# Optimization experiments

Hardware: AMD Instinct MI355X
Metric: run time of the kernel (lower is better)

Reference implementation:

```python
import jax, jax.numpy as jnp
import numpy as np

N = 4096
D_MODEL = 512


def setup_inputs() -> dict:
    key = jax.random.key(0)
    ks = jax.random.split(key, 5)
    scale = 1.0 / np.sqrt(D_MODEL)
    return {
        "x": jax.random.normal(ks[0], (N, D_MODEL), dtype=jnp.float32),
        "Wq": jax.random.normal(ks[1], (D_MODEL, D_MODEL), dtype=jnp.float32) * scale,
        "Wk": jax.random.normal(ks[2], (D_MODEL, D_MODEL), dtype=jnp.float32) * scale,
        "Wv": jax.random.normal(ks[3], (D_MODEL, D_MODEL), dtype=jnp.float32) * scale,
        "Ws": jax.random.normal(ks[4], (1, D_MODEL), dtype=jnp.float32) * scale,
    }


def reference(x, Wq, Wk, Wv, Ws):
    # x: [N, d]; torch nn.Linear(bias=False) computes x @ W.T
    Q = x @ Wq.T  # [N, d]
    K = x @ Wk.T  # [N, d]
    V = x @ Wv.T  # [N, d]
    sigma = jnp.clip(x @ Ws.T, 0.001, 1.0)  # [N, 1]

    # prior association: Gaussian kernel over |i - j| with per-row sigma
    pos = jnp.arange(sigma.shape[0], dtype=jnp.float32)
    diff = jnp.abs(pos[:, None] - pos[None, :])  # [N, N]
    gaussian = jnp.exp(-0.5 * (diff / sigma) ** 2) / jnp.sqrt(2.0 * jnp.pi * sigma)
    P = gaussian / (gaussian.sum(axis=1, keepdims=True) + 1e-8)

    scale = jnp.sqrt(jnp.float32(x.shape[-1]))
    S = jax.nn.softmax((Q @ K.T) / scale, axis=-1)  # [N, N]
    Z = S @ V  # [N, d]
    return Z, P, S
```

## Files before the change

### kernel.cpp

```cpp
#include <hip/hip_runtime.h>
#include <math.h>

#define N_TOK 4096
#define DM 512

typedef _Float16 f16x8 __attribute__((ext_vector_type(8)));
typedef _Float16 f16x4 __attribute__((ext_vector_type(4)));
typedef float f32x4 __attribute__((ext_vector_type(4)));

__device__ __forceinline__ void async_ld16(const ushort* g, ushort* l) {
  __builtin_amdgcn_global_load_lds(
      (const __attribute__((address_space(1))) void*)g,
      (__attribute__((address_space(3))) void*)l, 16, 0, 0);
}

__global__ __launch_bounds__(256) void pack_sigma(
    const float* __restrict__ x, const float* __restrict__ Wq,
    const float* __restrict__ Wk, const float* __restrict__ Wv,
    const float* __restrict__ Ws, _Float16* __restrict__ x16,
    _Float16* __restrict__ Wc16, float* __restrict__ sg) {
  const int b = blockIdx.x;
  const int t = threadIdx.x;
  if (b < 2048) {
    int i = b * 1024 + t * 4;
    float4 v = *(const float4*)&x[i];
    f16x4 o;
    o.x = (_Float16)v.x; o.y = (_Float16)v.y;
    o.z = (_Float16)v.z; o.w = (_Float16)v.w;
    *(f16x4*)&x16[i] = o;
    int col = (t * 4) & 511;
    float4 w = *(const float4*)&Ws[col];
    float p = v.x * w.x + v.y * w.y + v.z * w.z + v.w * w.w;
    __shared__ float red[256];
    red[t] = p;
    __syncthreads();
    int lt = t & 127;
    for (int off = 64; off > 0; off >>= 1) {
      if (lt < off) red[t] += red[t + off];
      __syncthreads();
    }
    if (lt == 0) {
      float s = red[t];
      sg[2 * b + (t >> 7)] = fminf(fmaxf(s, 0.001f), 1.0f);
    }
  } else {
    int e = (b - 2048) * 1024 + t * 4;
    const float* src;
    int le = e & (DM * DM - 1);
    if (e < DM * DM) src = Wq + le;
    else if (e < 2 * DM * DM) src = Wk + le;
    else src = Wv + le;
    float4 v = *(const float4*)src;
    f16x4 o;
    o.x = (_Float16)v.x; o.y = (_Float16)v.y;
    o.z = (_Float16)v.z; o.w = (_Float16)v.w;
    *(f16x4*)&Wc16[e] = o;
  }
}

template <int EPI>
__global__ __launch_bounds__(256) void mfma_f16(
    const _Float16* __restrict__ A, int lda, const _Float16* __restrict__ B,
    int ldb, int K, float scale, float* __restrict__ Cf, int ldc,
    _Float16* __restrict__ D0, _Float16* __restrict__ D1,
    _Float16* __restrict__ D2, float* __restrict__ Part) {
  __shared__ _Float16 lds[2 * 128 * 32];
  _Float16* Ah = lds;
  _Float16* Bh = lds + 128 * 32;

  const int t = threadIdx.x;
  const int w = t >> 6, L = t & 63;
  const int wm = (w >> 1) * 64, wn = (w & 1) * 64;
  const int row = L & 15, quad = L >> 4;
  const int bm = blockIdx.y * 128, bn = blockIdx.x * 128;
  const int kbase = blockIdx.z * K;

  f32x4 acc[4][4] = {{}};

  const int c0 = t, c1 = t + 256;
  const int r0 = c0 >> 2, o0 = (c0 & 3) * 8;
  const int r1 = r0 + 64;

  const ushort* ga0 = (const ushort*)(A + (size_t)(bm + r0) * lda + kbase + o0);
  const ushort* ga1 = (const ushort*)(A + (size_t)(bm + r1) * lda + kbase + o0);
  const ushort* gb0 = (const ushort*)(B + (size_t)(bn + r0) * ldb + kbase + o0);
  const ushort* gb1 = (const ushort*)(B + (size_t)(bn + r1) * ldb + kbase + o0);

  for (int k0 = 0; k0 < K; k0 += 32) {
    async_ld16(ga0, (ushort*)(Ah + c0 * 8));
    async_ld16(ga1, (ushort*)(Ah + c1 * 8));
    async_ld16(gb0, (ushort*)(Bh + c0 * 8));
    async_ld16(gb1, (ushort*)(Bh + c1 * 8));
    ga0 += 32; ga1 += 32; gb0 += 32; gb1 += 32;
    __syncthreads();

    f16x8 a0[4], b0[4];
#pragma unroll
    for (int i = 0; i < 4; ++i)
      a0[i] = *(const f16x8*)&Ah[(wm + i * 16 + row) * 32 + quad * 8];
#pragma unroll
    for (int j = 0; j < 4; ++j)
      b0[j] = *(const f16x8*)&Bh[(wn + j * 16 + row) * 32 + quad * 8];
#pragma unroll
    for (int i = 0; i < 4; ++i)
#pragma unroll
      for (int j = 0; j < 4; ++j)
        acc[i][j] = __builtin_amdgcn_mfma_f32_16x16x32_f16(a0[i], b0[j],
                                                           acc[i][j], 0, 0, 0);
    __syncthreads();
  }

  if (EPI == 1) {
    const int region = bn >> 9;
    _Float16* D = (region == 0) ? D0 : ((region == 1) ? D1 : D2);
#pragma unroll
    for (int i = 0; i < 4; ++i)
#pragma unroll
      for (int j = 0; j < 4; ++j)
#pragma unroll
        for (int r = 0; r < 4; ++r) {
          int gr = bm + wm + i * 16 + quad * 4 + r;
          int nn = (bn & 511) + wn + j * 16 + row;
          D[(size_t)gr * 512 + nn] = (_Float16)acc[i][j][r];
        }
  } else {
#pragma unroll
    for (int i = 0; i < 4; ++i)
#pragma unroll
      for (int j = 0; j < 4; ++j)
#pragma unroll
        for (int r = 0; r < 4; ++r) {
          int gr = bm + wm + i * 16 + quad * 4 + r;
          int gc = bn + wn + j * 16 + row;
          D0[(size_t)gr * ldc + gc] = (_Float16)(acc[i][j][r] * scale);
        }
  }
}

__global__ __launch_bounds__(256) void transpose16(
    const _Float16* __restrict__ V16, _Float16* __restrict__ VT) {
  __shared__ _Float16 T[32][34];
  const int t = threadIdx.x;
  const int r = t >> 3, c4 = (t & 7) * 4;
  f16x4 v = *(const f16x4*)&V16[(size_t)(blockIdx.y * 32 + r) * 512 +
                                blockIdx.x * 32 + c4];
  T[r][c4] = v.x; T[r][c4 + 1] = v.y; T[r][c4 + 2] = v.z; T[r][c4 + 3] = v.w;
  __syncthreads();
  f16x4 o;
  o.x = T[c4][r]; o.y = T[c4 + 1][r]; o.z = T[c4 + 2][r]; o.w = T[c4 + 3][r];
  *(f16x4*)&VT[(size_t)(blockIdx.x * 32 + r) * 4096 + blockIdx.y * 32 + c4] = o;
}

__global__ __launch_bounds__(256) void softmax_kernel(
    _Float16* __restrict__ Sc, float* __restrict__ S) {
  __shared__ float red[256];
  const int t = threadIdx.x;
  _Float16* Srow16 = Sc + (size_t)blockIdx.x * N_TOK;
  float* Srow = S + (size_t)blockIdx.x * N_TOK;
  float f[16];
  float m = -INFINITY;
#pragma unroll
  for (int r = 0; r < 4; ++r) {
    f16x4 h = *(const f16x4*)&Srow16[r * 1024 + t * 4];
    f[r * 4 + 0] = (float)h.x; f[r * 4 + 1] = (float)h.y;
    f[r * 4 + 2] = (float)h.z; f[r * 4 + 3] = (float)h.w;
    m = fmaxf(m, fmaxf(fmaxf(f[r * 4], f[r * 4 + 1]),
                       fmaxf(f[r * 4 + 2], f[r * 4 + 3])));
  }
  red[t] = m;
  __syncthreads();
  for (int off = 128; off > 0; off >>= 1) {
    if (t < off) red[t] = fmaxf(red[t], red[t + off]);
    __syncthreads();
  }
  m = red[0];
  __syncthreads();
  float sum = 0.f;
#pragma unroll
  for (int i = 0; i < 16; ++i) {
    f[i] = __expf(f[i] - m);
    sum += f[i];
  }
  red[t] = sum;
  __syncthreads();
  for (int off = 128; off > 0; off >>= 1) {
    if (t < off) red[t] += red[t + off];
    __syncthreads();
  }
  const float inv = 1.0f / red[0];
#pragma unroll
  for (int r = 0; r < 4; ++r) {
    float4 o;
    o.x = f[r * 4 + 0] * inv; o.y = f[r * 4 + 1] * inv;
    o.z = f[r * 4 + 2] * inv; o.w = f[r * 4 + 3] * inv;
    *(float4*)&Srow[r * 1024 + t * 4] = o;
    f16x4 h;
    h.x = (_Float16)o.x; h.y = (_Float16)o.y;
    h.z = (_Float16)o.z; h.w = (_Float16)o.w;
    *(f16x4*)&Srow16[r * 1024 + t * 4] = h;
  }
}

template <int FUSE_P>
__global__ __launch_bounds__(256) void sv_kernel(
    const _Float16* __restrict__ A,
    const _Float16* __restrict__ B,
    float* __restrict__ C,
    const float* __restrict__ sigma, float* __restrict__ P) {
  __shared__ _Float16 lds[2 * 64 * 32 + 2 * 128 * 32];
  const int t = threadIdx.x;

  if (FUSE_P && blockIdx.y >= 64) {
    float* red = (float*)lds;
    const int i = (blockIdx.y - 64) * 4 + blockIdx.x;
    const float sg = sigma[i];
    const float inv2 = -0.5f / (sg * sg);
    const float c = rsqrtf(6.283185307179586f * sg);
    float4 g[4];
    float sum = 0.f;
#pragma unroll
    for (int r = 0; r < 4; ++r) {
      int j = r * 1024 + t * 4;
      float d0 = (float)(i - j);
      float d1 = d0 - 1.f;
      float d2 = d0 - 2.f;
      float d3 = d0 - 3.f;
      g[r].x = __expf(inv2 * d0 * d0) * c;
      g[r].y = __expf(inv2 * d1 * d1) * c;
      g[r].z = __expf(inv2 * d2 * d2) * c;
      g[r].w = __expf(inv2 * d3 * d3) * c;
      sum += g[r].x + g[r].y + g[r].z + g[r].w;
    }
    red[t] = sum;
    __syncthreads();
    for (int off = 128; off > 0; off >>= 1) {
      if (t < off) red[t] += red[t + off];
      __syncthreads();
    }
    const float inv = 1.0f / (red[0] + 1e-8f);
    float* Prow = P + (size_t)i * N_TOK;
#pragma unroll
    for (int r = 0; r < 4; ++r) {
      g[r].x *= inv; g[r].y *= inv; g[r].z *= inv; g[r].w *= inv;
      *(float4*)&Prow[r * 1024 + t * 4] = g[r];
    }
    return;
  }

  _Float16* Ah = lds;
  _Float16* Bh = lds + 2 * 64 * 32;

  const int w = t >> 6, L = t & 63;
  const int wm = (w >> 1) * 32, wn = (w & 1) * 64;
  const int row = L & 15, quad = L >> 4;
  const int bm = blockIdx.y * 64, bn = blockIdx.x * 128;

  f32x4 acc[2][4] = {{}};

  const int rA = t >> 2, oA = (t & 3) * 8;
  const ushort* ga = (const ushort*)(A + (size_t)(bm + rA) * N_TOK + oA);
  const ushort* gb0 = (const ushort*)(B + (size_t)(bn + rA) * N_TOK + oA);
  const ushort* gb1 = (const ushort*)(B + (size_t)(bn + rA + 64) * N_TOK + oA);

  for (int k0 = 0; k0 < N_TOK; k0 += 64) {
    async_ld16(ga, (ushort*)(Ah + t * 8));
    async_ld16(ga + 32, (ushort*)(Ah + 2048 + t * 8));
    async_ld16(gb0, (ushort*)(Bh + t * 8));
    async_ld16(gb1, (ushort*)(Bh + (t + 256) * 8));
    async_ld16(gb0 + 32, (ushort*)(Bh + 4096 + t * 8));
    async_ld16(gb1 + 32, (ushort*)(Bh + 4096 + (t + 256) * 8));
    ga += 64; gb0 += 64; gb1 += 64;
    __syncthreads();

    f16x8 a0[2][2], b0[2][4];
#pragma unroll
    for (int kk = 0; kk < 2; ++kk) {
#pragma unroll
      for (int i = 0; i < 2; ++i)
        a0[kk][i] =
            *(const f16x8*)&Ah[kk * 2048 + (wm + i * 16 + row) * 32 + quad * 8];
#pragma unroll
      for (int j = 0; j < 4; ++j)
        b0[kk][j] =
            *(const f16x8*)&Bh[kk * 4096 + (wn + j * 16 + row) * 32 + quad * 8];
    }
#pragma unroll
    for (int kk = 0; kk < 2; ++kk)
#pragma unroll
      for (int i = 0; i < 2; ++i)
#pragma unroll
        for (int j = 0; j < 4; ++j)
          acc[i][j] = __builtin_amdgcn_mfma_f32_16x16x32_f16(
              a0[kk][i], b0[kk][j], acc[i][j], 0, 0, 0);
    __syncthreads();
  }

#pragma unroll
  for (int i = 0; i < 2; ++i)
#pragma unroll
    for (int j = 0; j < 4; ++j)
#pragma unroll
      for (int r = 0; r < 4; ++r) {
        int gr = bm + wm + i * 16 + quad * 4 + r;
        int gc = bn + wn + j * 16 + row;
        C[(size_t)gr * 512 + gc] = acc[i][j][r];
      }
}

__global__ __launch_bounds__(256) void tailP(const float* __restrict__ sigma,
                                             float* __restrict__ P) {
  __shared__ float red[256];
  const int t = threadIdx.x;
  const int i = blockIdx.x;
  const float sg = sigma[i];
  const float inv2 = -0.5f / (sg * sg);
  const float c = rsqrtf(6.283185307179586f * sg);
  float4 g[4];
  float sum = 0.f;
#pragma unroll
  for (int r = 0; r < 4; ++r) {
    int j = r * 1024 + t * 4;
    float d0 = (float)(i - j);
    float d1 = d0 - 1.f;
    float d2 = d0 - 2.f;
    float d3 = d0 - 3.f;
    g[r].x = __expf(inv2 * d0 * d0) * c;
    g[r].y = __expf(inv2 * d1 * d1) * c;
    g[r].z = __expf(inv2 * d2 * d2) * c;
    g[r].w = __expf(inv2 * d3 * d3) * c;
    sum += g[r].x + g[r].y + g[r].z + g[r].w;
  }
  red[t] = sum;
  __syncthreads();
  for (int off = 128; off > 0; off >>= 1) {
    if (t < off) red[t] += red[t + off];
    __syncthreads();
  }
  const float inv = 1.0f / (red[0] + 1e-8f);
  float* Prow = P + (size_t)i * N_TOK;
#pragma unroll
  for (int r = 0; r < 4; ++r) {
    g[r].x *= inv; g[r].y *= inv; g[r].z *= inv; g[r].w *= inv;
    *(float4*)&Prow[r * 1024 + t * 4] = g[r];
  }
}

extern "C" void kernel_launch(void* const* d_in, const int* in_sizes, int n_in,
                              void* d_out, int out_size, void* d_ws,
                              size_t ws_size, hipStream_t stream) {
  const float* x = (const float*)d_in[0];
  const float* Wq = (const float*)d_in[1];
  const float* Wk = (const float*)d_in[2];
  const float* Wv = (const float*)d_in[3];
  const float* Ws = (const float*)d_in[4];

  float* out = (float*)d_out;
  float* Z = out;
  float* Pout = Z + (size_t)N_TOK * DM;
  float* S = Pout + (size_t)N_TOK * N_TOK;

  const size_t E = (size_t)N_TOK * DM;

  _Float16* x16 = (_Float16*)d_ws;
  _Float16* Wc16 = x16 + E;
  float* sg = (float*)(Wc16 + 3 * DM * DM);
  _Float16* stage = (_Float16*)(sg + 4096);

  const size_t stage_bytes = (4 * E + (size_t)N_TOK * N_TOK) * sizeof(_Float16);
  const size_t base_bytes = (size_t)((char*)stage - (char*)d_ws);
  const bool ws_ok = ws_size >= base_bytes + stage_bytes;

  _Float16* Q16 = ws_ok ? stage : (_Float16*)Pout;
  _Float16* K16 = Q16 + E;
  _Float16* V16 = K16 + E;
  _Float16* VT16 = V16 + E;
  _Float16* Sc16 = VT16 + E;

  const dim3 blk(256);

  pack_sigma<<<2816, blk, 0, stream>>>(x, Wq, Wk, Wv, Ws, x16, Wc16, sg);

  mfma_f16<1><<<dim3(12, 32), blk, 0, stream>>>(
      x16, DM, Wc16, DM, DM, 1.0f, nullptr, 0, Q16, K16, V16, nullptr);

  transpose16<<<dim3(16, 128), blk, 0, stream>>>(V16, VT16);

  mfma_f16<3><<<dim3(32, 32), blk, 0, stream>>>(
      Q16, DM, K16, DM, DM, 1.0f / sqrtf((float)DM), nullptr, N_TOK, Sc16,
      nullptr, nullptr, nullptr);

  softmax_kernel<<<N_TOK, blk, 0, stream>>>(Sc16, S);

  if (ws_ok) {
    sv_kernel<1><<<dim3(4, 64 + 1024), blk, 0, stream>>>(Sc16, VT16, Z, sg,
                                                         Pout);
  } else {
    sv_kernel<0><<<dim3(4, 64), blk, 0, stream>>>(Sc16, VT16, Z, nullptr,
                                                  nullptr);
    tailP<<<N_TOK, blk, 0, stream>>>(sg, Pout);
  }
}
```

Baseline: 267.1 us.

## Unify GEMMs into triple-buffered async-load pipeline with larger QK tiles

```diff
diff --git a/kernel.cpp b/kernel.cpp
--- a/kernel.cpp
+++ b/kernel.cpp
@@ -12,6 +12,11 @@
   __builtin_amdgcn_global_load_lds(
       (const __attribute__((address_space(1))) void*)g,
       (__attribute__((address_space(3))) void*)l, 16, 0, 0);
+}
+
+template <int N>
+__device__ __forceinline__ void vm_wait() {
+  asm volatile("s_waitcnt vmcnt(%0)" ::"i"(N) : "memory");
 }
 
 __global__ __launch_bounds__(256) void pack_sigma(
@@ -58,81 +63,162 @@
   }
 }
 
-template <int EPI>
-__global__ __launch_bounds__(256) void mfma_f16(
+template <int BM, int BN, int BK, int NT, int EPI, int FUSE_P>
+__global__ __launch_bounds__(256) void gemm_pipe(
     const _Float16* __restrict__ A, int lda, const _Float16* __restrict__ B,
-    int ldb, int K, float scale, float* __restrict__ Cf, int ldc,
-    _Float16* __restrict__ D0, _Float16* __restrict__ D1,
-    _Float16* __restrict__ D2, float* __restrict__ Part) {
-  __shared__ _Float16 lds[2 * 128 * 32];
-  _Float16* Ah = lds;
-  _Float16* Bh = lds + 128 * 32;
-
-  const int t = threadIdx.x;
-  const int w = t >> 6, L = t & 63;
-  const int wm = (w >> 1) * 64, wn = (w & 1) * 64;
-  const int row = L & 15, quad = L >> 4;
-  const int bm = blockIdx.y * 128, bn = blockIdx.x * 128;
-  const int kbase = blockIdx.z * K;
-
-  f32x4 acc[4][4] = {{}};
-
-  const int c0 = t, c1 = t + 256;
-  const int r0 = c0 >> 2, o0 = (c0 & 3) * 8;
-  const int r1 = r0 + 64;
-
-  const ushort* ga0 = (const ushort*)(A + (size_t)(bm + r0) * lda + kbase + o0);
-  const ushort* ga1 = (const ushort*)(A + (size_t)(bm + r1) * lda + kbase + o0);
-  const ushort* gb0 = (const ushort*)(B + (size_t)(bn + r0) * ldb + kbase + o0);
-  const ushort* gb1 = (const ushort*)(B + (size_t)(bn + r1) * ldb + kbase + o0);
-
-  for (int k0 = 0; k0 < K; k0 += 32) {
-    async_ld16(ga0, (ushort*)(Ah + c0 * 8));
-    async_ld16(ga1, (ushort*)(Ah + c1 * 8));
-    async_ld16(gb0, (ushort*)(Bh + c0 * 8));
-    async_ld16(gb1, (ushort*)(Bh + c1 * 8));
-    ga0 += 32; ga1 += 32; gb0 += 32; gb1 += 32;
-    __syncthreads();
-
-    f16x8 a0[4], b0[4];
-#pragma unroll
-    for (int i = 0; i < 4; ++i)
-      a0[i] = *(const f16x8*)&Ah[(wm + i * 16 + row) * 32 + quad * 8];
-#pragma unroll
-    for (int j = 0; j < 4; ++j)
-      b0[j] = *(const f16x8*)&Bh[(wn + j * 16 + row) * 32 + quad * 8];
-#pragma unroll
-    for (int i = 0; i < 4; ++i)
-#pragma unroll
-      for (int j = 0; j < 4; ++j)
-        acc[i][j] = __builtin_amdgcn_mfma_f32_16x16x32_f16(a0[i], b0[j],
-                                                           acc[i][j], 0, 0, 0);
-    __syncthreads();
-  }
-
-  if (EPI == 1) {
+    int ldb, float scale, float* __restrict__ Cf, _Float16* __restrict__ D0,
+    _Float16* __restrict__ D1, _Float16* __restrict__ D2,
+    const float* __restrict__ sigma, float* __restrict__ P) {
+  constexpr int TB = (BM + BN) * BK;
+  constexpr int ACH = BM * BK / 8;
+  constexpr int BCH = BN * BK / 8;
+  constexpr int L = (ACH + BCH) / 256;
+  constexpr int MI = BM / 32;
+  constexpr int NJ = BN / 32;
+  __shared__ _Float16 lds[3 * TB];
+  const int t = threadIdx.x;
+
+  if (FUSE_P && blockIdx.y >= 64) {
+    float* red = (float*)lds;
+    const int pidx = (blockIdx.y - 64) * 4 + blockIdx.x;
+    const int w = t >> 6, lane = t & 63;
+#pragma unroll 1
+    for (int rr = 0; rr < 4; ++rr) {
+      const int i = pidx * 4 + rr;
+      const float sgv = sigma[i];
+      const float inv2 = -0.5f / (sgv * sgv);
+      const float cc = rsqrtf(6.283185307179586f * sgv);
+      float4 g[4];
+      float sum = 0.f;
+#pragma unroll
+      for (int r = 0; r < 4; ++r) {
+        int j = r * 1024 + t * 4;
+        float d0 = (float)(i - j);
+        float d1 = d0 - 1.f, d2 = d0 - 2.f, d3 = d0 - 3.f;
+        g[r].x = __expf(inv2 * d0 * d0) * cc;
+        g[r].y = __expf(inv2 * d1 * d1) * cc;
+        g[r].z = __expf(inv2 * d2 * d2) * cc;
+        g[r].w = __expf(inv2 * d3 * d3) * cc;
+        sum += g[r].x + g[r].y + g[r].z + g[r].w;
+      }
+#pragma unroll
+      for (int off = 32; off > 0; off >>= 1) sum += __shfl_xor(sum, off);
+      if (lane == 0) red[w] = sum;
+      __syncthreads();
+      const float inv = 1.0f / (red[0] + red[1] + red[2] + red[3] + 1e-8f);
+      float* Prow = P + (size_t)i * N_TOK;
+#pragma unroll
+      for (int r = 0; r < 4; ++r) {
+        g[r].x *= inv; g[r].y *= inv; g[r].z *= inv; g[r].w *= inv;
+        *(float4*)&Prow[r * 1024 + t * 4] = g[r];
+      }
+      __syncthreads();
+    }
+    return;
+  }
+
+  const int w = t >> 6, Ln = t & 63;
+  const int wm = (w >> 1) * (BM / 2), wn = (w & 1) * (BN / 2);
+  const int row = Ln & 15, quad = Ln >> 4;
+  const int bm = blockIdx.y * BM, bn = blockIdx.x * BN;
+
+  f32x4 acc[MI][NJ] = {{}};
+
+  const ushort* gp[L];
+#pragma unroll
+  for (int k = 0; k < L; ++k) {
+    int c = t + k * 256;
+    if (c < ACH) {
+      int r = c / (BK / 8), c8 = c % (BK / 8);
+      gp[k] = (const ushort*)(A + (size_t)(bm + r) * lda + c8 * 8);
+    } else {
+      int cb = c - ACH;
+      int r = cb / (BK / 8), c8 = cb % (BK / 8);
+      gp[k] = (const ushort*)(B + (size_t)(bn + r) * ldb + c8 * 8);
+    }
+  }
+
+  auto stage = [&](int buf) {
+    _Float16* dst = lds + buf * TB;
+#pragma unroll
+    for (int k = 0; k < L; ++k) {
+      async_ld16(gp[k], (ushort*)(dst + (t + k * 256) * 8));
+      gp[k] += BK;
+    }
+  };
+
+  stage(0);
+  stage(1);
+
+  for (int tt = 0; tt < NT; ++tt) {
+    const int cur = tt % 3;
+    if (tt + 2 < NT) stage((tt + 2) % 3);
+    if (tt < NT - 2) vm_wait<2 * L>();
+    else if (tt == NT - 2) vm_wait<L>();
+    else vm_wait<0>();
+    __builtin_amdgcn_s_barrier();
+
+    const _Float16* Ah = lds + cur * TB;
+    const _Float16* Bh = Ah + BM * BK;
+    f16x8 af[BK / 32][MI], bf[BK / 32][NJ];
+#pragma unroll
+    for (int kk = 0; kk < BK / 32; ++kk) {
+#pragma unroll
+      for (int i = 0; i < MI; ++i)
+        af[kk][i] =
+            *(const f16x8*)&Ah[(wm + i * 16 + row) * BK + kk * 32 + quad * 8];
+#pragma unroll
+      for (int j = 0; j < NJ; ++j)
+        bf[kk][j] =
+            *(const f16x8*)&Bh[(wn + j * 16 + row) * BK + kk * 32 + quad * 8];
+    }
+#pragma unroll
+    for (int kk = 0; kk < BK / 32; ++kk)
+#pragma unroll
+      for (int i = 0; i < MI; ++i)
+#pragma unroll
+        for (int j = 0; j < NJ; ++j)
+          acc[i][j] = __builtin_amdgcn_mfma_f32_16x16x32_f16(
+              af[kk][i], bf[kk][j], acc[i][j], 0, 0, 0);
+
+    asm volatile("s_waitcnt lgkmcnt(0)" ::: "memory");
+    __builtin_amdgcn_s_barrier();
+  }
+
+  if constexpr (EPI == 1) {
     const int region = bn >> 9;
     _Float16* D = (region == 0) ? D0 : ((region == 1) ? D1 : D2);
 #pragma unroll
-    for (int i = 0; i < 4; ++i)
-#pragma unroll
-      for (int j = 0; j < 4; ++j)
+    for (int i = 0; i < MI; ++i)
+#pragma unroll
+      for (int j = 0; j < NJ; ++j)
 #pragma unroll
         for (int r = 0; r < 4; ++r) {
           int gr = bm + wm + i * 16 + quad * 4 + r;
           int nn = (bn & 511) + wn + j * 16 + row;
           D[(size_t)gr * 512 + nn] = (_Float16)acc[i][j][r];
         }
-  } else {
-#pragma unroll
-    for (int i = 0; i < 4; ++i)
-#pragma unroll
-      for (int j = 0; j < 4; ++j)
+  } else if constexpr (EPI == 3) {
+#pragma unroll
+    for (int i = 0; i < MI; ++i)
+#pragma unroll
+      for (int j = 0; j < NJ; ++j)
 #pragma unroll
         for (int r = 0; r < 4; ++r) {
           int gr = bm + wm + i * 16 + quad * 4 + r;
           int gc = bn + wn + j * 16 + row;
-          D0[(size_t)gr * ldc + gc] = (_Float16)(acc[i][j][r] * scale);
+          D0[(size_t)gr * N_TOK + gc] = (_Float16)(acc[i][j][r] * scale);
+        }
+  } else {
+#pragma unroll
+    for (int i = 0; i < MI; ++i)
+#pragma unroll
+      for (int j = 0; j < NJ; ++j)
+#pragma unroll
+        for (int r = 0; r < 4; ++r) {
+          int gr = bm + wm + i * 16 + quad * 4 + r;
+          int gc = bn + wn + j * 16 + row;
+          Cf[(size_t)gr * DM + gc] = acc[i][j][r];
         }
   }
 }
@@ -201,112 +287,6 @@
   }
 }
 
-template <int FUSE_P>
-__global__ __launch_bounds__(256) void sv_kernel(
-    const _Float16* __restrict__ A,
-    const _Float16* __restrict__ B,
-    float* __restrict__ C,
-    const float* __restrict__ sigma, float* __restrict__ P) {
-  __shared__ _Float16 lds[2 * 64 * 32 + 2 * 128 * 32];
-  const int t = threadIdx.x;
-
-  if (FUSE_P && blockIdx.y >= 64) {
-    float* red = (float*)lds;
-    const int i = (blockIdx.y - 64) * 4 + blockIdx.x;
-    const float sg = sigma[i];
-    const float inv2 = -0.5f / (sg * sg);
-    const float c = rsqrtf(6.283185307179586f * sg);
-    float4 g[4];
-    float sum = 0.f;
-#pragma unroll
-    for (int r = 0; r < 4; ++r) {
-      int j = r * 1024 + t * 4;
-      float d0 = (float)(i - j);
-      float d1 = d0 - 1.f;
-      float d2 = d0 - 2.f;
-      float d3 = d0 - 3.f;
-      g[r].x = __expf(inv2 * d0 * d0) * c;
-      g[r].y = __expf(inv2 * d1 * d1) * c;
-      g[r].z = __expf(inv2 * d2 * d2) * c;
-      g[r].w = __expf(inv2 * d3 * d3) * c;
-      sum += g[r].x + g[r].y + g[r].z + g[r].w;
-    }
-    red[t] = sum;
-    __syncthreads();
-    for (int off = 128; off > 0; off >>= 1) {
-      if (t < off) red[t] += red[t + off];
-      __syncthreads();
-    }
-    const float inv = 1.0f / (red[0] + 1e-8f);
-    float* Prow = P + (size_t)i * N_TOK;
-#pragma unroll
-    for (int r = 0; r < 4; ++r) {
-      g[r].x *= inv; g[r].y *= inv; g[r].z *= inv; g[r].w *= inv;
-      *(float4*)&Prow[r * 1024 + t * 4] = g[r];
-    }
-    return;
-  }
-
-  _Float16* Ah = lds;
-  _Float16* Bh = lds + 2 * 64 * 32;
-
-  const int w = t >> 6, L = t & 63;
-  const int wm = (w >> 1) * 32, wn = (w & 1) * 64;
-  const int row = L & 15, quad = L >> 4;
-  const int bm = blockIdx.y * 64, bn = blockIdx.x * 128;
-
-  f32x4 acc[2][4] = {{}};
-
-  const int rA = t >> 2, oA = (t & 3) * 8;
-  const ushort* ga = (const ushort*)(A + (size_t)(bm + rA) * N_TOK + oA);
-  const ushort* gb0 = (const ushort*)(B + (size_t)(bn + rA) * N_TOK + oA);
-  const ushort* gb1 = (const ushort*)(B + (size_t)(bn + rA + 64) * N_TOK + oA);
-
-  for (int k0 = 0; k0 < N_TOK; k0 += 64) {
-    async_ld16(ga, (ushort*)(Ah + t * 8));
-    async_ld16(ga + 32, (ushort*)(Ah + 2048 + t * 8));
-    async_ld16(gb0, (ushort*)(Bh + t * 8));
-    async_ld16(gb1, (ushort*)(Bh + (t + 256) * 8));
-    async_ld16(gb0 + 32, (ushort*)(Bh + 4096 + t * 8));
-    async_ld16(gb1 + 32, (ushort*)(Bh + 4096 + (t + 256) * 8));
-    ga += 64; gb0 += 64; gb1 += 64;
-    __syncthreads();
-
-    f16x8 a0[2][2], b0[2][4];
-#pragma unroll
-    for (int kk = 0; kk < 2; ++kk) {
-#pragma unroll
-      for (int i = 0; i < 2; ++i)
-        a0[kk][i] =
-            *(const f16x8*)&Ah[kk * 2048 + (wm + i * 16 + row) * 32 + quad * 8];
-#pragma unroll
-      for (int j = 0; j < 4; ++j)
-        b0[kk][j] =
-            *(const f16x8*)&Bh[kk * 4096 + (wn + j * 16 + row) * 32 + quad * 8];
-    }
-#pragma unroll
-    for (int kk = 0; kk < 2; ++kk)
-#pragma unroll
-      for (int i = 0; i < 2; ++i)
-#pragma unroll
-        for (int j = 0; j < 4; ++j)
-          acc[i][j] = __builtin_amdgcn_mfma_f32_16x16x32_f16(
-              a0[kk][i], b0[kk][j], acc[i][j], 0, 0, 0);
-    __syncthreads();
-  }
-
-#pragma unroll
-  for (int i = 0; i < 2; ++i)
-#pragma unroll
-    for (int j = 0; j < 4; ++j)
-#pragma unroll
-      for (int r = 0; r < 4; ++r) {
-        int gr = bm + wm + i * 16 + quad * 4 + r;
-        int gc = bn + wn + j * 16 + row;
-        C[(size_t)gr * 512 + gc] = acc[i][j][r];
-      }
-}
-
 __global__ __launch_bounds__(256) void tailP(const float* __restrict__ sigma,
                                              float* __restrict__ P) {
   __shared__ float red[256];
@@ -321,9 +301,7 @@
   for (int r = 0; r < 4; ++r) {
     int j = r * 1024 + t * 4;
     float d0 = (float)(i - j);
-    float d1 = d0 - 1.f;
-    float d2 = d0 - 2.f;
-    float d3 = d0 - 3.f;
+    float d1 = d0 - 1.f, d2 = d0 - 2.f, d3 = d0 - 3.f;
     g[r].x = __expf(inv2 * d0 * d0) * c;
     g[r].y = __expf(inv2 * d1 * d1) * c;
     g[r].z = __expf(inv2 * d2 * d2) * c;
@@ -377,26 +355,28 @@
   _Float16* Sc16 = VT16 + E;
 
   const dim3 blk(256);
+  const float qk_scale = 1.0f / sqrtf((float)DM);
 
   pack_sigma<<<2816, blk, 0, stream>>>(x, Wq, Wk, Wv, Ws, x16, Wc16, sg);
 
-  mfma_f16<1><<<dim3(12, 32), blk, 0, stream>>>(
-      x16, DM, Wc16, DM, DM, 1.0f, nullptr, 0, Q16, K16, V16, nullptr);
+  gemm_pipe<128, 128, 32, 16, 1, 0><<<dim3(12, 32), blk, 0, stream>>>(
+      x16, DM, Wc16, DM, 1.0f, nullptr, Q16, K16, V16, nullptr, nullptr);
 
   transpose16<<<dim3(16, 128), blk, 0, stream>>>(V16, VT16);
 
-  mfma_f16<3><<<dim3(32, 32), blk, 0, stream>>>(
-      Q16, DM, K16, DM, DM, 1.0f / sqrtf((float)DM), nullptr, N_TOK, Sc16,
-      nullptr, nullptr, nullptr);
+  gemm_pipe<256, 128, 32, 16, 3, 0><<<dim3(32, 16), blk, 0, stream>>>(
+      Q16, DM, K16, DM, qk_scale, nullptr, Sc16, nullptr, nullptr, nullptr,
+      nullptr);
 
   softmax_kernel<<<N_TOK, blk, 0, stream>>>(Sc16, S);
 
   if (ws_ok) {
-    sv_kernel<1><<<dim3(4, 64 + 1024), blk, 0, stream>>>(Sc16, VT16, Z, sg,
-                                                         Pout);
+    gemm_pipe<64, 128, 64, 64, 2, 1><<<dim3(4, 64 + 256), blk, 0, stream>>>(
+        Sc16, N_TOK, VT16, N_TOK, 1.0f, Z, nullptr, nullptr, nullptr, sg, Pout);
   } else {
-    sv_kernel<0><<<dim3(4, 64), blk, 0, stream>>>(Sc16, VT16, Z, nullptr,
-                                                  nullptr);
+    gemm_pipe<64, 128, 64, 64, 2, 0><<<dim3(4, 64), blk, 0, stream>>>(
+        Sc16, N_TOK, VT16, N_TOK, 1.0f, Z, nullptr, nullptr, nullptr, nullptr,
+        nullptr);
     tailP<<<N_TOK, blk, 0, stream>>>(sg, Pout);
   }
 }
```

After: 244.6 us. -8.5%, faster.
